# Optimization experiments

Measured on AMD Instinct MI355X. Metric: run time of the kernel, lower is better.

The kernel has to match this reference:

```python
import jax, jax.numpy as jnp
import numpy as np

EMB = 512
HID = 1024
BATCH = 64
TX = 512


def setup_inputs() -> dict:
    key = jax.random.key(0)
    ks = jax.random.split(key, 9)
    s = 0.05
    return {
        "word": jax.random.normal(ks[0], (BATCH, TX, EMB), dtype=jnp.float32),
        "Wz": jax.random.normal(ks[1], (HID, HID + EMB), dtype=jnp.float32) * s,
        "bz": jax.random.normal(ks[2], (HID,), dtype=jnp.float32) * s,
        "Wr": jax.random.normal(ks[3], (HID, HID + EMB), dtype=jnp.float32) * s,
        "br": jax.random.normal(ks[4], (HID,), dtype=jnp.float32) * s,
        "Wh": jax.random.normal(ks[5], (HID, HID + EMB), dtype=jnp.float32) * s,
        "bh": jax.random.normal(ks[6], (HID,), dtype=jnp.float32) * s,
        "Wy": jax.random.normal(ks[7], (EMB, HID), dtype=jnp.float32) * s,
        "by": jax.random.normal(ks[8], (EMB,), dtype=jnp.float32) * s,
    }


def reference(word, Wz, bz, Wr, br, Wh, bh, Wy, by):
    batch = word.shape[0]
    word_t = jnp.transpose(word, (1, 0, 2))  # [T, B, E]
    h0 = jnp.zeros((batch, HID), dtype=word.dtype)
    x0 = jnp.zeros((batch, EMB), dtype=word.dtype)

    def step(carry, w_i):
        h, x = carry  # x is the PREVIOUS timestep's word (lags by one, as in the torch code)
        comb = jnp.concatenate([h, x], axis=1)  # [B, HID+EMB]
        z = jax.nn.sigmoid(comb @ Wz.T + bz)
        r = jax.nn.sigmoid(comb @ Wr.T + br)
        comb2 = jnp.concatenate([r * h, x], axis=1)
        h_tilde = jnp.tanh(comb2 @ Wh.T + bh)
        h_new = (1.0 - z) * h + z * h_tilde
        y = h_new @ Wy.T + by  # [B, E]
        return (h_new, w_i), y

    _, ys = jax.lax.scan(step, (h0, x0), word_t)  # ys: [T, B, E]
    return jnp.transpose(ys, (1, 0, 2))  # [B, T, E]
```

## Files before the change

### kernel.cpp

```cpp
#include <hip/hip_runtime.h>
#include <hip/hip_bf16.h>


#define EMB 512
#define HID 1024
#define BATCHN 64
#define TLEN 512
#define CAT 1536
#define GROUPS 4
#define GB 16
#define WPG 32
#define HX_LD 1032
#define ZL_LD 34
#define GPAD 8

typedef __attribute__((ext_vector_type(8))) short bf16x8;
typedef __attribute__((ext_vector_type(4))) short s16x4;
typedef __attribute__((ext_vector_type(4))) float f32x4;
typedef unsigned int u32;
typedef unsigned long long u64;
typedef unsigned short u16;

__device__ __forceinline__ float bf2f(u16 u) {
  union { float f; u32 i; } v; v.i = ((u32)u) << 16; return v.f;
}
__device__ __forceinline__ u16 f2bf(float f) {
  union { float f; u32 i; } v; v.f = f;
  u32 r = v.i + 0x7fffu + ((v.i >> 16) & 1u);
  return (u16)(r >> 16);
}

__device__ __forceinline__ u64 ld_dc(const u16* p) {
  return __hip_atomic_load((const u64*)p, __ATOMIC_RELAXED, __HIP_MEMORY_SCOPE_AGENT);
}
__device__ __forceinline__ void st_dc16(u16* p, u16 v) {
  __hip_atomic_store(p, v, __ATOMIC_RELAXED, __HIP_MEMORY_SCOPE_AGENT);
}

__global__ __launch_bounds__(256) void convert_gate_w(const float* __restrict__ W,
                                                      u16* __restrict__ Wh_,
                                                      u16* __restrict__ Wx_) {
  int i = blockIdx.x * 256 + threadIdx.x;
  if (i >= HID * CAT) return;
  int row = i / CAT, col = i - row * CAT;
  u16 v = f2bf(W[i]);
  if (col < HID) Wh_[row * HID + col] = v;
  else           Wx_[row * EMB + (col - HID)] = v;
}

__global__ __launch_bounds__(256) void convert_wy(const float* __restrict__ W, u16* __restrict__ Wy_) {
  int i = blockIdx.x * 256 + threadIdx.x;
  if (i < EMB * HID) Wy_[i] = f2bf(W[i]);
}

__global__ __launch_bounds__(256) void proj_kernel(const float* __restrict__ word,
                                                   const u16* __restrict__ Wx,
                                                   const float* __restrict__ bias,
                                                   u16* __restrict__ P) {
  __shared__ __align__(16) u16 As[64][64 + GPAD];
  __shared__ __align__(16) u16 Bs[64][64 + GPAD];
  const int tid = threadIdx.x;
  const int wid = tid >> 6, lane = tid & 63;
  const int m0 = blockIdx.x * 64, n0 = blockIdx.y * 64;
  const int mw = (wid >> 1) * 32, nw = (wid & 1) * 32;
  f32x4 acc[2][2] = {};
  for (int k0 = 0; k0 < EMB; k0 += 64) {
#pragma unroll
    for (int it = 0; it < 4; ++it) {
      int e = (it * 256 + tid) * 4;
      int row = e >> 6, col = e & 63;
      int R = m0 + row;
      float4 a = make_float4(0.f, 0.f, 0.f, 0.f);
      if ((R & (TLEN - 1)) != 0)
        a = *reinterpret_cast<const float4*>(&word[(u64)(R - 1) * EMB + k0 + col]);
      s16x4 vv;
      vv[0] = (short)f2bf(a.x); vv[1] = (short)f2bf(a.y);
      vv[2] = (short)f2bf(a.z); vv[3] = (short)f2bf(a.w);
      *reinterpret_cast<s16x4*>(&As[row][col]) = vv;
    }
#pragma unroll
    for (int it = 0; it < 2; ++it) {
      int e = (it * 256 + tid) * 8;
      int row = e >> 6, col = e & 63;
      *reinterpret_cast<bf16x8*>(&Bs[row][col]) =
          *reinterpret_cast<const bf16x8*>(&Wx[(u64)(n0 + row) * EMB + k0 + col]);
    }
    __syncthreads();
#pragma unroll
    for (int kk = 0; kk < 2; ++kk) {
      const int kb = kk * 32 + 8 * (lane >> 4);
#pragma unroll
      for (int i = 0; i < 2; ++i) {
        bf16x8 a = *reinterpret_cast<const bf16x8*>(&As[mw + i * 16 + (lane & 15)][kb]);
#pragma unroll
        for (int j = 0; j < 2; ++j) {
          bf16x8 b = *reinterpret_cast<const bf16x8*>(&Bs[nw + j * 16 + (lane & 15)][kb]);
          acc[i][j] = __builtin_amdgcn_mfma_f32_16x16x32_bf16(a, b, acc[i][j], 0, 0, 0);
        }
      }
    }
    __syncthreads();
  }
#pragma unroll
  for (int i = 0; i < 2; ++i)
#pragma unroll
    for (int j = 0; j < 2; ++j) {
      int col = n0 + nw + j * 16 + (lane & 15);
      float bv = bias[col];
#pragma unroll
      for (int q = 0; q < 4; ++q) {
        int row = m0 + mw + i * 16 + 4 * (lane >> 4) + q;
        P[(u64)row * HID + col] = f2bf(acc[i][j][q] + bv);
      }
    }
}

__global__ __launch_bounds__(256) void out_gemm(const u16* __restrict__ H,
                                                const u16* __restrict__ Wy,
                                                const float* __restrict__ by,
                                                float* __restrict__ out) {
  __shared__ __align__(16) u16 As[64][64 + GPAD];
  __shared__ __align__(16) u16 Bs[64][64 + GPAD];
  const int tid = threadIdx.x;
  const int wid = tid >> 6, lane = tid & 63;
  const int m0 = blockIdx.x * 64, n0 = blockIdx.y * 64;
  const int mw = (wid >> 1) * 32, nw = (wid & 1) * 32;
  f32x4 acc[2][2] = {};
  for (int k0 = 0; k0 < HID; k0 += 64) {
#pragma unroll
    for (int it = 0; it < 2; ++it) {
      int e = (it * 256 + tid) * 8;
      int row = e >> 6, col = e & 63;
      *reinterpret_cast<bf16x8*>(&As[row][col]) =
          *reinterpret_cast<const bf16x8*>(&H[(u64)(m0 + row) * HID + k0 + col]);
      *reinterpret_cast<bf16x8*>(&Bs[row][col]) =
          *reinterpret_cast<const bf16x8*>(&Wy[(u64)(n0 + row) * HID + k0 + col]);
    }
    __syncthreads();
#pragma unroll
    for (int kk = 0; kk < 2; ++kk) {
      const int kb = kk * 32 + 8 * (lane >> 4);
#pragma unroll
      for (int i = 0; i < 2; ++i) {
        bf16x8 a = *reinterpret_cast<const bf16x8*>(&As[mw + i * 16 + (lane & 15)][kb]);
#pragma unroll
        for (int j = 0; j < 2; ++j) {
          bf16x8 b = *reinterpret_cast<const bf16x8*>(&Bs[nw + j * 16 + (lane & 15)][kb]);
          acc[i][j] = __builtin_amdgcn_mfma_f32_16x16x32_bf16(a, b, acc[i][j], 0, 0, 0);
        }
      }
    }
    __syncthreads();
  }
#pragma unroll
  for (int i = 0; i < 2; ++i)
#pragma unroll
    for (int j = 0; j < 2; ++j) {
      int col = n0 + nw + j * 16 + (lane & 15);
      float bv = by[col];
#pragma unroll
      for (int q = 0; q < 4; ++q) {
        int row = m0 + mw + i * 16 + 4 * (lane >> 4) + q;
        out[(u64)row * EMB + col] = acc[i][j][q] + bv;
      }
    }
}

__device__ __forceinline__ void group_barrier(u32* gflags, int rank, u32 target) {
  __syncthreads();
  asm volatile("" ::: "memory");
  if (threadIdx.x < 64) {
    if ((int)threadIdx.x == rank)
      __hip_atomic_store(&gflags[rank * 16], target, __ATOMIC_RELAXED, __HIP_MEMORY_SCOPE_AGENT);
    const int active = (threadIdx.x < WPG) ? 1 : 0;
    u32* addr = &gflags[((int)threadIdx.x & (WPG - 1)) * 16];
    for (;;) {
      u32 v = __hip_atomic_load(addr, __ATOMIC_RELAXED, __HIP_MEMORY_SCOPE_AGENT);
      if (!__any(active & ((v < target) ? 1 : 0))) break;
      __builtin_amdgcn_s_sleep(1);
    }
  }
  __syncthreads();
  asm volatile("" ::: "memory");
}

__global__ __launch_bounds__(256, 1) void gru_persistent(
    const u16* __restrict__ Wzh, const u16* __restrict__ Wrh, const u16* __restrict__ Whh,
    const u16* __restrict__ Pz, const u16* __restrict__ Pr, u16* __restrict__ PhH,
    u16* __restrict__ rhbuf, u32* flags) {
  __shared__ __align__(16) u16 hx[16 * HX_LD];
  __shared__ __align__(16) u16 zL[16 * ZL_LD];
  __shared__ __align__(16) float RED[4 * 64 * 4];

  const int tid = threadIdx.x;
  const int wid = tid >> 6;
  const int lane = tid & 63;
  const int l15 = lane & 15;
  const int k4 = lane >> 4;
  const int g = blockIdx.x & (GROUPS - 1);
  const int w = blockIdx.x >> 2;
  const int b0 = g * GB;
  const int j = wid & 1;
  const int gate = wid >> 1;
  const int kh = wid >> 1;
  const int colA = 32 * w + 16 * j + l15;
  const u16* __restrict__ PA = gate ? Pr : Pz;
  u32* gflags = flags + g * (WPG * 16);

  const int srow = tid >> 4;
  const int soff = (tid & 15) * 4;

  bf16x8 wfA[32];
#pragma unroll
  for (int s = 0; s < 32; ++s)
    wfA[s] = *reinterpret_cast<const bf16x8*>(
        (gate ? Wrh : Wzh) + (u64)colA * HID + 32 * s + k4 * 8);
  bf16x8 wfB[16];
#pragma unroll
  for (int s = 0; s < 16; ++s)
    wfB[s] = *reinterpret_cast<const bf16x8*>(
        Whh + (u64)colA * HID + kh * 512 + 32 * s + k4 * 8);
#pragma unroll
  for (int s = 0; s < 32; ++s) asm volatile("" : "+v"(wfA[s]));
#pragma unroll
  for (int s = 0; s < 16; ++s) asm volatile("" : "+v"(wfB[s]));

  for (int e = tid; e < 16 * HX_LD / 2; e += 256) reinterpret_cast<u32*>(hx)[e] = 0u;
  __syncthreads();

  float pAc[4], pBc[4];
#pragma unroll
  for (int q = 0; q < 4; ++q) {
    int m = 4 * k4 + q;
    pAc[q] = bf2f(PA[((u64)(b0 + m) * TLEN) * HID + colA]);
    pBc[q] = bf2f(PhH[((u64)(b0 + m) * TLEN) * HID + colA]);
  }

  float hprev[4] = {0.f, 0.f, 0.f, 0.f};
  u32 ph = 0;

  for (int t = 0; t < TLEN; ++t) {
    if (t > 0) {
      const u16* src = PhH + ((u64)(b0 + srow) * TLEN + (t - 1)) * HID + soff;
      u64 tmp[16];
#pragma unroll
      for (int i = 0; i < 16; ++i) tmp[i] = ld_dc(src + i * 64);
      u16* dst = &hx[srow * HX_LD + soff];
#pragma unroll
      for (int i = 0; i < 16; ++i) *reinterpret_cast<u64*>(dst + i * 64) = tmp[i];
      __syncthreads();
    }

    f32x4 acc = {0.f, 0.f, 0.f, 0.f}, acc_b = {0.f, 0.f, 0.f, 0.f};
    if (t > 0) {
#pragma unroll
      for (int s = 0; s < 32; s += 2) {
        bf16x8 a0 = *reinterpret_cast<const bf16x8*>(&hx[l15 * HX_LD + 32 * s + k4 * 8]);
        bf16x8 a1 = *reinterpret_cast<const bf16x8*>(&hx[l15 * HX_LD + 32 * (s + 1) + k4 * 8]);
        acc   = __builtin_amdgcn_mfma_f32_16x16x32_bf16(a0, wfA[s],     acc,   0, 0, 0);
        acc_b = __builtin_amdgcn_mfma_f32_16x16x32_bf16(a1, wfA[s + 1], acc_b, 0, 0, 0);
      }
    }
#pragma unroll
    for (int q = 0; q < 4; ++q) {
      int m = 4 * k4 + q;
      float pre = acc[q] + acc_b[q] + pAc[q];
      float sg = 1.f / (1.f + __expf(-pre));
      if (gate == 0) {
        zL[m * ZL_LD + 16 * j + l15] = f2bf(sg);
      } else {
        st_dc16(rhbuf + (u64)(g * GB + m) * HID + colA, f2bf(sg * hprev[q]));
      }
    }
    group_barrier(gflags, w, ++ph);

    {
      const u16* src = rhbuf + (u64)(g * GB + srow) * HID + soff;
      u64 tmp[16];
#pragma unroll
      for (int i = 0; i < 16; ++i) tmp[i] = ld_dc(src + i * 64);
      u16* dst = &hx[srow * HX_LD + soff];
#pragma unroll
      for (int i = 0; i < 16; ++i) *reinterpret_cast<u64*>(dst + i * 64) = tmp[i];
      __syncthreads();
    }

    f32x4 acc2 = {0.f, 0.f, 0.f, 0.f}, acc2b = {0.f, 0.f, 0.f, 0.f};
#pragma unroll
    for (int s = 0; s < 16; s += 2) {
      bf16x8 a0 = *reinterpret_cast<const bf16x8*>(
          &hx[l15 * HX_LD + kh * 512 + 32 * s + k4 * 8]);
      bf16x8 a1 = *reinterpret_cast<const bf16x8*>(
          &hx[l15 * HX_LD + kh * 512 + 32 * (s + 1) + k4 * 8]);
      acc2  = __builtin_amdgcn_mfma_f32_16x16x32_bf16(a0, wfB[s],     acc2,  0, 0, 0);
      acc2b = __builtin_amdgcn_mfma_f32_16x16x32_bf16(a1, wfB[s + 1], acc2b, 0, 0, 0);
    }
#pragma unroll
    for (int q = 0; q < 4; ++q) acc2[q] += acc2b[q];
    *reinterpret_cast<f32x4*>(&RED[(wid * 64 + lane) * 4]) = acc2;
    __syncthreads();
    {
      f32x4 part = *reinterpret_cast<const f32x4*>(&RED[((wid ^ 2) * 64 + lane) * 4]);
#pragma unroll
      for (int q = 0; q < 4; ++q) {
        int m = 4 * k4 + q;
        float pre = acc2[q] + part[q] + pBc[q];
        float e2 = __expf(2.f * pre);
        float th = 1.f - 2.f / (e2 + 1.f);
        float zq = bf2f(zL[m * ZL_LD + 16 * j + l15]);
        float hn = (1.f - zq) * hprev[q] + zq * th;
        hprev[q] = hn;
        if (wid < 2)
          st_dc16(PhH + ((u64)(b0 + m) * TLEN + t) * HID + colA, f2bf(hn));
      }
    }
    {
      int tn = (t + 1 < TLEN) ? (t + 1) : t;
#pragma unroll
      for (int q = 0; q < 4; ++q) {
        int m = 4 * k4 + q;
        pAc[q] = bf2f(PA[((u64)(b0 + m) * TLEN + tn) * HID + colA]);
        pBc[q] = bf2f(PhH[((u64)(b0 + m) * TLEN + tn) * HID + colA]);
      }
    }
    group_barrier(gflags, w, ++ph);
  }
}

extern "C" void kernel_launch(void* const* d_in, const int* in_sizes, int n_in,
                              void* d_out, int out_size, void* d_ws, size_t ws_size,
                              hipStream_t stream) {
  const float* word = (const float*)d_in[0];
  const float* Wz = (const float*)d_in[1];
  const float* bz = (const float*)d_in[2];
  const float* Wr = (const float*)d_in[3];
  const float* br = (const float*)d_in[4];
  const float* Wh = (const float*)d_in[5];
  const float* bh = (const float*)d_in[6];
  const float* Wy = (const float*)d_in[7];
  const float* by = (const float*)d_in[8];
  float* out = (float*)d_out;
  (void)in_sizes; (void)n_in; (void)out_size; (void)ws_size;

  char* ws = (char*)d_ws;
  size_t off = 0;
  auto alloc = [&](size_t bytes) {
    char* p = ws + off;
    off += (bytes + 255) & ~(size_t)255;
    return p;
  };
  u32* flags = (u32*)alloc(GROUPS * WPG * 16 * sizeof(u32));
  u16* WzhB = (u16*)alloc((size_t)HID * HID * 2);
  u16* WrhB = (u16*)alloc((size_t)HID * HID * 2);
  u16* WhhB = (u16*)alloc((size_t)HID * HID * 2);
  u16* WzxB = (u16*)alloc((size_t)HID * EMB * 2);
  u16* WrxB = (u16*)alloc((size_t)HID * EMB * 2);
  u16* WhxB = (u16*)alloc((size_t)HID * EMB * 2);
  u16* WyB  = (u16*)alloc((size_t)EMB * HID * 2);
  u16* Pr   = (u16*)alloc((size_t)BATCHN * TLEN * HID * 2);
  u16* PhH  = (u16*)alloc((size_t)BATCHN * TLEN * HID * 2);
  u16* rhbuf = (u16*)alloc((size_t)GROUPS * GB * HID * 2);
  u16* Pz = (u16*)d_out;

  hipMemsetAsync(flags, 0, GROUPS * WPG * 16 * sizeof(u32), stream);

  convert_gate_w<<<(HID * CAT + 255) / 256, 256, 0, stream>>>(Wz, WzhB, WzxB);
  convert_gate_w<<<(HID * CAT + 255) / 256, 256, 0, stream>>>(Wr, WrhB, WrxB);
  convert_gate_w<<<(HID * CAT + 255) / 256, 256, 0, stream>>>(Wh, WhhB, WhxB);
  convert_wy<<<(EMB * HID + 255) / 256, 256, 0, stream>>>(Wy, WyB);

  dim3 pg(512, 16);
  proj_kernel<<<pg, 256, 0, stream>>>(word, WzxB, bz, Pz);
  proj_kernel<<<pg, 256, 0, stream>>>(word, WrxB, br, Pr);
  proj_kernel<<<pg, 256, 0, stream>>>(word, WhxB, bh, PhH);

  gru_persistent<<<dim3(GROUPS * WPG), dim3(256), 0, stream>>>(WzhB, WrhB, WhhB, Pz, Pr, PhH,
                                                               rhbuf, flags);

  out_gemm<<<dim3(512, 8), 256, 0, stream>>>(PhH, WyB, by, out);
}
```

Measured before the change: 3.093 ms.

## Replace flag barriers with epoch-tagged data words in double-buffered exchange buffers

```diff
diff --git a/kernel.cpp b/kernel.cpp
--- a/kernel.cpp
+++ b/kernel.cpp
@@ -30,10 +30,10 @@
   return (u16)(r >> 16);
 }
 
-__device__ __forceinline__ u64 ld_dc(const u16* p) {
+__device__ __forceinline__ u64 ld_dc64(const u32* p) {
   return __hip_atomic_load((const u64*)p, __ATOMIC_RELAXED, __HIP_MEMORY_SCOPE_AGENT);
 }
-__device__ __forceinline__ void st_dc16(u16* p, u16 v) {
+__device__ __forceinline__ void st_dc32(u32* p, u32 v) {
   __hip_atomic_store(p, v, __ATOMIC_RELAXED, __HIP_MEMORY_SCOPE_AGENT);
 }
 
@@ -166,28 +166,10 @@
     }
 }
 
-__device__ __forceinline__ void group_barrier(u32* gflags, int rank, u32 target) {
-  __syncthreads();
-  asm volatile("" ::: "memory");
-  if (threadIdx.x < 64) {
-    if ((int)threadIdx.x == rank)
-      __hip_atomic_store(&gflags[rank * 16], target, __ATOMIC_RELAXED, __HIP_MEMORY_SCOPE_AGENT);
-    const int active = (threadIdx.x < WPG) ? 1 : 0;
-    u32* addr = &gflags[((int)threadIdx.x & (WPG - 1)) * 16];
-    for (;;) {
-      u32 v = __hip_atomic_load(addr, __ATOMIC_RELAXED, __HIP_MEMORY_SCOPE_AGENT);
-      if (!__any(active & ((v < target) ? 1 : 0))) break;
-      __builtin_amdgcn_s_sleep(1);
-    }
-  }
-  __syncthreads();
-  asm volatile("" ::: "memory");
-}
-
 __global__ __launch_bounds__(256, 1) void gru_persistent(
     const u16* __restrict__ Wzh, const u16* __restrict__ Wrh, const u16* __restrict__ Whh,
     const u16* __restrict__ Pz, const u16* __restrict__ Pr, u16* __restrict__ PhH,
-    u16* __restrict__ rhbuf, u32* flags) {
+    u32* __restrict__ rhbuf32, u32* __restrict__ hxbuf32) {
   __shared__ __align__(16) u16 hx[16 * HX_LD];
   __shared__ __align__(16) u16 zL[16 * ZL_LD];
   __shared__ __align__(16) float RED[4 * 64 * 4];
@@ -205,10 +187,9 @@
   const int kh = wid >> 1;
   const int colA = 32 * w + 16 * j + l15;
   const u16* __restrict__ PA = gate ? Pr : Pz;
-  u32* gflags = flags + g * (WPG * 16);
 
   const int srow = tid >> 4;
-  const int soff = (tid & 15) * 4;
+  const int soff = (tid & 15) * 2;
 
   bf16x8 wfA[32];
 #pragma unroll
@@ -224,9 +205,6 @@
   for (int s = 0; s < 32; ++s) asm volatile("" : "+v"(wfA[s]));
 #pragma unroll
   for (int s = 0; s < 16; ++s) asm volatile("" : "+v"(wfB[s]));
-
-  for (int e = tid; e < 16 * HX_LD / 2; e += 256) reinterpret_cast<u32*>(hx)[e] = 0u;
-  __syncthreads();
 
   float pAc[4], pBc[4];
 #pragma unroll
@@ -237,17 +215,31 @@
   }
 
   float hprev[4] = {0.f, 0.f, 0.f, 0.f};
-  u32 ph = 0;
 
   for (int t = 0; t < TLEN; ++t) {
+    const int par = t & 1;
+    const u32 epN = (u32)(t + 1);
+
     if (t > 0) {
-      const u16* src = PhH + ((u64)(b0 + srow) * TLEN + (t - 1)) * HID + soff;
-      u64 tmp[16];
-#pragma unroll
-      for (int i = 0; i < 16; ++i) tmp[i] = ld_dc(src + i * 64);
+      const u32 ep = (u32)t;
+      const u32* src = hxbuf32 + (u64)((t - 1) & 1) * (BATCHN * HID) +
+                       (u64)(b0 + srow) * HID + soff;
+      u64 tmp[32];
+      for (;;) {
+        bool ok = true;
+#pragma unroll
+        for (int i = 0; i < 32; ++i) tmp[i] = ld_dc64(src + i * 32);
+#pragma unroll
+        for (int i = 0; i < 32; ++i)
+          ok &= (((u32)(tmp[i] >> 16) & 0xFFFFu) == ep) & ((u32)(tmp[i] >> 48) == ep);
+        if (ok) break;
+      }
       u16* dst = &hx[srow * HX_LD + soff];
 #pragma unroll
-      for (int i = 0; i < 16; ++i) *reinterpret_cast<u64*>(dst + i * 64) = tmp[i];
+      for (int i = 0; i < 32; ++i) {
+        u32 packed = (u32)(tmp[i] & 0xFFFFu) | (((u32)(tmp[i] >> 32) & 0xFFFFu) << 16);
+        *reinterpret_cast<u32*>(dst + i * 32) = packed;
+      }
       __syncthreads();
     }
 
@@ -269,19 +261,31 @@
       if (gate == 0) {
         zL[m * ZL_LD + 16 * j + l15] = f2bf(sg);
       } else {
-        st_dc16(rhbuf + (u64)(g * GB + m) * HID + colA, f2bf(sg * hprev[q]));
-      }
-    }
-    group_barrier(gflags, w, ++ph);
+        u32 pv = (u32)f2bf(sg * hprev[q]) | (epN << 16);
+        st_dc32(rhbuf32 + (u64)par * (BATCHN * HID) + (u64)(b0 + m) * HID + colA, pv);
+      }
+    }
+    __syncthreads();
 
     {
-      const u16* src = rhbuf + (u64)(g * GB + srow) * HID + soff;
-      u64 tmp[16];
-#pragma unroll
-      for (int i = 0; i < 16; ++i) tmp[i] = ld_dc(src + i * 64);
+      const u32* src = rhbuf32 + (u64)par * (BATCHN * HID) +
+                       (u64)(b0 + srow) * HID + soff;
+      u64 tmp[32];
+      for (;;) {
+        bool ok = true;
+#pragma unroll
+        for (int i = 0; i < 32; ++i) tmp[i] = ld_dc64(src + i * 32);
+#pragma unroll
+        for (int i = 0; i < 32; ++i)
+          ok &= (((u32)(tmp[i] >> 16) & 0xFFFFu) == epN) & ((u32)(tmp[i] >> 48) == epN);
+        if (ok) break;
+      }
       u16* dst = &hx[srow * HX_LD + soff];
 #pragma unroll
-      for (int i = 0; i < 16; ++i) *reinterpret_cast<u64*>(dst + i * 64) = tmp[i];
+      for (int i = 0; i < 32; ++i) {
+        u32 packed = (u32)(tmp[i] & 0xFFFFu) | (((u32)(tmp[i] >> 32) & 0xFFFFu) << 16);
+        *reinterpret_cast<u32*>(dst + i * 32) = packed;
+      }
       __syncthreads();
     }
 
@@ -310,8 +314,12 @@
         float zq = bf2f(zL[m * ZL_LD + 16 * j + l15]);
         float hn = (1.f - zq) * hprev[q] + zq * th;
         hprev[q] = hn;
-        if (wid < 2)
-          st_dc16(PhH + ((u64)(b0 + m) * TLEN + t) * HID + colA, f2bf(hn));
+        if (wid < 2) {
+          u16 hb = f2bf(hn);
+          st_dc32(hxbuf32 + (u64)par * (BATCHN * HID) + (u64)(b0 + m) * HID + colA,
+                  (u32)hb | (epN << 16));
+          PhH[((u64)(b0 + m) * TLEN + t) * HID + colA] = hb;
+        }
       }
     }
     {
@@ -323,7 +331,6 @@
         pBc[q] = bf2f(PhH[((u64)(b0 + m) * TLEN + tn) * HID + colA]);
       }
     }
-    group_barrier(gflags, w, ++ph);
   }
 }
 
@@ -349,7 +356,8 @@
     off += (bytes + 255) & ~(size_t)255;
     return p;
   };
-  u32* flags = (u32*)alloc(GROUPS * WPG * 16 * sizeof(u32));
+  u32* rhbuf32 = (u32*)alloc((size_t)2 * BATCHN * HID * 4);
+  u32* hxbuf32 = (u32*)alloc((size_t)2 * BATCHN * HID * 4);
   u16* WzhB = (u16*)alloc((size_t)HID * HID * 2);
   u16* WrhB = (u16*)alloc((size_t)HID * HID * 2);
   u16* WhhB = (u16*)alloc((size_t)HID * HID * 2);
@@ -359,10 +367,9 @@
   u16* WyB  = (u16*)alloc((size_t)EMB * HID * 2);
   u16* Pr   = (u16*)alloc((size_t)BATCHN * TLEN * HID * 2);
   u16* PhH  = (u16*)alloc((size_t)BATCHN * TLEN * HID * 2);
-  u16* rhbuf = (u16*)alloc((size_t)GROUPS * GB * HID * 2);
   u16* Pz = (u16*)d_out;
 
-  hipMemsetAsync(flags, 0, GROUPS * WPG * 16 * sizeof(u32), stream);
+  hipMemsetAsync(rhbuf32, 0, (size_t)4 * BATCHN * HID * 4, stream);
 
   convert_gate_w<<<(HID * CAT + 255) / 256, 256, 0, stream>>>(Wz, WzhB, WzxB);
   convert_gate_w<<<(HID * CAT + 255) / 256, 256, 0, stream>>>(Wr, WrhB, WrxB);
@@ -375,7 +382,7 @@
   proj_kernel<<<pg, 256, 0, stream>>>(word, WhxB, bh, PhH);
 
   gru_persistent<<<dim3(GROUPS * WPG), dim3(256), 0, stream>>>(WzhB, WrhB, WhhB, Pz, Pr, PhH,
-                                                               rhbuf, flags);
+                                                               rhbuf32, hxbuf32);
 
   out_gemm<<<dim3(512, 8), 256, 0, stream>>>(PhH, WyB, by, out);
 }
```

Result: slower. 3.990 ms (+29.0%).

## Split group barrier into signal/poll, overlap preloads, and XOR-swizzle hx shared layout

Applied to the files above, without the earlier changes.

```diff
diff --git a/kernel.cpp b/kernel.cpp
--- a/kernel.cpp
+++ b/kernel.cpp
@@ -10,7 +10,7 @@
 #define GROUPS 4
 #define GB 16
 #define WPG 32
-#define HX_LD 1032
+#define HX_LD 1024
 #define ZL_LD 34
 #define GPAD 8
 
@@ -166,22 +166,14 @@
     }
 }
 
-__device__ __forceinline__ void group_barrier(u32* gflags, int rank, u32 target) {
-  __syncthreads();
-  asm volatile("" ::: "memory");
+__device__ __forceinline__ void poll_flags(u32* gflags, u32 target) {
   if (threadIdx.x < 64) {
-    if ((int)threadIdx.x == rank)
-      __hip_atomic_store(&gflags[rank * 16], target, __ATOMIC_RELAXED, __HIP_MEMORY_SCOPE_AGENT);
-    const int active = (threadIdx.x < WPG) ? 1 : 0;
     u32* addr = &gflags[((int)threadIdx.x & (WPG - 1)) * 16];
     for (;;) {
       u32 v = __hip_atomic_load(addr, __ATOMIC_RELAXED, __HIP_MEMORY_SCOPE_AGENT);
-      if (!__any(active & ((v < target) ? 1 : 0))) break;
-      __builtin_amdgcn_s_sleep(1);
+      if (!__any((int)(v < target))) break;
     }
   }
-  __syncthreads();
-  asm volatile("" ::: "memory");
 }
 
 __global__ __launch_bounds__(256, 1) void gru_persistent(
@@ -207,8 +199,11 @@
   const u16* __restrict__ PA = gate ? Pr : Pz;
   u32* gflags = flags + g * (WPG * 16);
 
+  const int sw = (l15 & 7) << 3;
+
   const int srow = tid >> 4;
   const int soff = (tid & 15) * 4;
+  const int ssw = (srow & 7) << 3;
 
   bf16x8 wfA[32];
 #pragma unroll
@@ -245,9 +240,10 @@
       u64 tmp[16];
 #pragma unroll
       for (int i = 0; i < 16; ++i) tmp[i] = ld_dc(src + i * 64);
-      u16* dst = &hx[srow * HX_LD + soff];
-#pragma unroll
-      for (int i = 0; i < 16; ++i) *reinterpret_cast<u64*>(dst + i * 64) = tmp[i];
+      u16* dst = &hx[srow * HX_LD];
+#pragma unroll
+      for (int i = 0; i < 16; ++i)
+        *reinterpret_cast<u64*>(dst + ((soff + i * 64) ^ ssw)) = tmp[i];
       __syncthreads();
     }
 
@@ -255,8 +251,10 @@
     if (t > 0) {
 #pragma unroll
       for (int s = 0; s < 32; s += 2) {
-        bf16x8 a0 = *reinterpret_cast<const bf16x8*>(&hx[l15 * HX_LD + 32 * s + k4 * 8]);
-        bf16x8 a1 = *reinterpret_cast<const bf16x8*>(&hx[l15 * HX_LD + 32 * (s + 1) + k4 * 8]);
+        bf16x8 a0 = *reinterpret_cast<const bf16x8*>(
+            &hx[l15 * HX_LD + ((32 * s + k4 * 8) ^ sw)]);
+        bf16x8 a1 = *reinterpret_cast<const bf16x8*>(
+            &hx[l15 * HX_LD + ((32 * (s + 1) + k4 * 8) ^ sw)]);
         acc   = __builtin_amdgcn_mfma_f32_16x16x32_bf16(a0, wfA[s],     acc,   0, 0, 0);
         acc_b = __builtin_amdgcn_mfma_f32_16x16x32_bf16(a1, wfA[s + 1], acc_b, 0, 0, 0);
       }
@@ -272,16 +270,33 @@
         st_dc16(rhbuf + (u64)(g * GB + m) * HID + colA, f2bf(sg * hprev[q]));
       }
     }
-    group_barrier(gflags, w, ++ph);
+
+    ++ph;
+    __syncthreads();
+    asm volatile("" ::: "memory");
+    if (tid == w)
+      __hip_atomic_store(&gflags[w * 16], ph, __ATOMIC_RELAXED, __HIP_MEMORY_SCOPE_AGENT);
+    {
+      int tn = (t + 1 < TLEN) ? (t + 1) : t;
+#pragma unroll
+      for (int q = 0; q < 4; ++q) {
+        int m = 4 * k4 + q;
+        pAc[q] = bf2f(PA[((u64)(b0 + m) * TLEN + tn) * HID + colA]);
+      }
+    }
+    poll_flags(gflags, ph);
+    __syncthreads();
+    asm volatile("" ::: "memory");
 
     {
       const u16* src = rhbuf + (u64)(g * GB + srow) * HID + soff;
       u64 tmp[16];
 #pragma unroll
       for (int i = 0; i < 16; ++i) tmp[i] = ld_dc(src + i * 64);
-      u16* dst = &hx[srow * HX_LD + soff];
-#pragma unroll
-      for (int i = 0; i < 16; ++i) *reinterpret_cast<u64*>(dst + i * 64) = tmp[i];
+      u16* dst = &hx[srow * HX_LD];
+#pragma unroll
+      for (int i = 0; i < 16; ++i)
+        *reinterpret_cast<u64*>(dst + ((soff + i * 64) ^ ssw)) = tmp[i];
       __syncthreads();
     }
 
@@ -289,9 +304,9 @@
 #pragma unroll
     for (int s = 0; s < 16; s += 2) {
       bf16x8 a0 = *reinterpret_cast<const bf16x8*>(
-          &hx[l15 * HX_LD + kh * 512 + 32 * s + k4 * 8]);
+          &hx[l15 * HX_LD + ((kh * 512 + 32 * s + k4 * 8) ^ sw)]);
       bf16x8 a1 = *reinterpret_cast<const bf16x8*>(
-          &hx[l15 * HX_LD + kh * 512 + 32 * (s + 1) + k4 * 8]);
+          &hx[l15 * HX_LD + ((kh * 512 + 32 * (s + 1) + k4 * 8) ^ sw)]);
       acc2  = __builtin_amdgcn_mfma_f32_16x16x32_bf16(a0, wfB[s],     acc2,  0, 0, 0);
       acc2b = __builtin_amdgcn_mfma_f32_16x16x32_bf16(a1, wfB[s + 1], acc2b, 0, 0, 0);
     }
@@ -314,16 +329,23 @@
           st_dc16(PhH + ((u64)(b0 + m) * TLEN + t) * HID + colA, f2bf(hn));
       }
     }
+
+    ++ph;
+    __syncthreads();
+    asm volatile("" ::: "memory");
+    if (tid == w)
+      __hip_atomic_store(&gflags[w * 16], ph, __ATOMIC_RELAXED, __HIP_MEMORY_SCOPE_AGENT);
     {
       int tn = (t + 1 < TLEN) ? (t + 1) : t;
 #pragma unroll
       for (int q = 0; q < 4; ++q) {
         int m = 4 * k4 + q;
-        pAc[q] = bf2f(PA[((u64)(b0 + m) * TLEN + tn) * HID + colA]);
         pBc[q] = bf2f(PhH[((u64)(b0 + m) * TLEN + tn) * HID + colA]);
       }
     }
-    group_barrier(gflags, w, ++ph);
+    poll_flags(gflags, ph);
+    __syncthreads();
+    asm volatile("" ::: "memory");
   }
 }
 
```

After: 2.941 ms. -4.9%, faster.
